# Optimization experiments

Hardware: AMD Instinct MI355X
Metric: run time of the kernel (lower is better)

## Reference

```python
import jax, jax.numpy as jnp
import numpy as np

DIM = 1024
HEADS = 16
HIDDEN = 4096
EPS = 1e-5


def layernorm(x, w, b):
    mu = jnp.mean(x, axis=-1, keepdims=True)
    var = jnp.var(x, axis=-1, keepdims=True)
    return (x - mu) * jax.lax.rsqrt(var + EPS) * w + b


def setup_inputs() -> dict:
    key = jax.random.key(0)
    ks = jax.random.split(key, 12)
    s = lambda fan_in: 1.0 / np.sqrt(fan_in)
    return {
        "x": jax.random.normal(ks[0], (8, 1024, DIM), dtype=jnp.float32),
        "norm1_w": jnp.ones((DIM,), jnp.float32),
        "norm1_b": jnp.zeros((DIM,), jnp.float32),
        "qkv_w": jax.random.uniform(ks[1], (3 * DIM, DIM), jnp.float32, -s(DIM), s(DIM)),
        "proj_w": jax.random.uniform(ks[2], (DIM, DIM), jnp.float32, -s(DIM), s(DIM)),
        "proj_b": jax.random.uniform(ks[3], (DIM,), jnp.float32, -s(DIM), s(DIM)),
        "norm2_w": jnp.ones((DIM,), jnp.float32),
        "norm2_b": jnp.zeros((DIM,), jnp.float32),
        "fc1_w": jax.random.uniform(ks[4], (HIDDEN, DIM), jnp.float32, -s(DIM), s(DIM)),
        "fc1_b": jax.random.uniform(ks[5], (HIDDEN,), jnp.float32, -s(DIM), s(DIM)),
        "fc2_w": jax.random.uniform(ks[6], (DIM, HIDDEN), jnp.float32, -s(HIDDEN), s(HIDDEN)),
        "fc2_b": jax.random.uniform(ks[7], (DIM,), jnp.float32, -s(HIDDEN), s(HIDDEN)),
    }


def reference(x, norm1_w, norm1_b, qkv_w, proj_w, proj_b,
              norm2_w, norm2_b, fc1_w, fc1_b, fc2_w, fc2_b):
    B, N, C = x.shape
    hd = C // HEADS
    scale = hd ** -0.5

    # ---- attention branch ----
    xn = layernorm(x, norm1_w, norm1_b)
    qkv_tmp = jnp.einsum('bnc,oc->bno', xn, qkv_w)          # [B,N,3C]
    qkv = qkv_tmp.reshape(B, N, 3, HEADS, hd).transpose(2, 0, 3, 1, 4)
    q, k, v = qkv[0], qkv[1], qkv[2]                         # [B,H,N,hd]
    qkv_out = qkv_tmp.reshape(B, N, 3, C).transpose(2, 0, 1, 3)
    attn = jnp.einsum('bhnd,bhmd->bhnm', q, k) * scale       # [B,H,N,N]
    attn = jax.nn.softmax(attn, axis=-1)
    ao = jnp.einsum('bhnm,bhmd->bhnd', attn, v)              # [B,H,N,hd]
    ao = ao.transpose(0, 2, 1, 3).reshape(B, N, C)
    attn_out = jnp.einsum('bnc,oc->bno', ao, proj_w) + proj_b
    x = x + attn_out

    # ---- mlp branch ----
    xn2 = layernorm(x, norm2_w, norm2_b)
    h = jnp.einsum('bnc,hc->bnh', xn2, fc1_w) + fc1_b
    h = jax.nn.gelu(h, approximate=False)
    hidden_out = jnp.einsum('bnh,ch->bnc', h, fc2_w) + fc2_b
    x = x + hidden_out
    return (x, (qkv_out[0], qkv_out[1], qkv_out[2]), hidden_out)
```

## Files before the change

### kernel.cpp

```cpp
#include <hip/hip_runtime.h>
#include <hip/hip_bf16.h>

typedef __attribute__((ext_vector_type(8))) __bf16 bf16x8;
typedef __attribute__((ext_vector_type(4))) float f32x4;
typedef unsigned short u16;
typedef unsigned int u32;

#define TOK 8192
#define C_DIM 1024
#define OUT_SEC 8388608

__device__ __forceinline__ u16 f2bf(float f) {
  return __builtin_bit_cast(u16, __float2bfloat16(f));
}

__device__ __forceinline__ int cvt_pk_bf16(float lo, float hi) {
  int r;
  asm("v_cvt_pk_bf16_f32 %0, %1, %2" : "=v"(r) : "v"(lo), "v"(hi));
  return r;
}

__device__ __forceinline__ float max3f(float a, float b, float c) {
  return fmaxf(fmaxf(a, b), c);
}

__device__ __forceinline__ void gl_lds16(const void* g, void* l) {
  __builtin_amdgcn_global_load_lds(
      (__attribute__((address_space(1))) void*)const_cast<void*>(g),
      (__attribute__((address_space(3))) void*)l, 16, 0, 0);
}

__device__ __forceinline__ float gelu_f(float x) {
  float y = 0.7978845608f * (x + 0.044715f * x * x * x);
  y = fminf(fmaxf(y, -15.f), 15.f);
  float e = __expf(2.0f * y);
  float th = (e - 1.0f) / (e + 1.0f);
  return 0.5f * x * (1.0f + th);
}

__global__ __launch_bounds__(256) void cvt_kernel(const float* __restrict__ in,
                                                  u16* __restrict__ out, int n4) {
  int i = blockIdx.x * blockDim.x + threadIdx.x;
  if (i >= n4) return;
  float4 v = reinterpret_cast<const float4*>(in)[i];
  alignas(8) u16 pk[4];
  pk[0] = f2bf(v.x); pk[1] = f2bf(v.y); pk[2] = f2bf(v.z); pk[3] = f2bf(v.w);
  reinterpret_cast<uint2*>(out)[i] = *reinterpret_cast<uint2*>(pk);
}

__global__ __launch_bounds__(256) void ln_kernel(const float* __restrict__ x,
                                                 const float* __restrict__ w,
                                                 const float* __restrict__ b,
                                                 u16* __restrict__ out) {
  const int row = blockIdx.x;
  const int t = threadIdx.x;
  const float* xr = x + (size_t)row * C_DIM;
  float4 v = reinterpret_cast<const float4*>(xr)[t];
  float s = v.x + v.y + v.z + v.w;
  float ss = v.x * v.x + v.y * v.y + v.z * v.z + v.w * v.w;
#pragma unroll
  for (int off = 1; off < 64; off <<= 1) {
    s += __shfl_xor(s, off, 64);
    ss += __shfl_xor(ss, off, 64);
  }
  __shared__ float red[8];
  const int wv = t >> 6;
  if ((t & 63) == 0) { red[wv] = s; red[4 + wv] = ss; }
  __syncthreads();
  s = red[0] + red[1] + red[2] + red[3];
  ss = red[4] + red[5] + red[6] + red[7];
  const float mu = s * (1.0f / C_DIM);
  const float var = ss * (1.0f / C_DIM) - mu * mu;
  const float rstd = rsqrtf(var + 1e-5f);
  float4 w4 = reinterpret_cast<const float4*>(w)[t];
  float4 b4 = reinterpret_cast<const float4*>(b)[t];
  alignas(8) u16 pk[4];
  pk[0] = f2bf((v.x - mu) * rstd * w4.x + b4.x);
  pk[1] = f2bf((v.y - mu) * rstd * w4.y + b4.y);
  pk[2] = f2bf((v.z - mu) * rstd * w4.z + b4.z);
  pk[3] = f2bf((v.w - mu) * rstd * w4.w + b4.w);
  reinterpret_cast<uint2*>(out + (size_t)row * C_DIM)[t] = *reinterpret_cast<uint2*>(pk);
}

__global__ __launch_bounds__(256) void vtrans_kernel(const float* __restrict__ vsrc,
                                                     u16* __restrict__ vt) {
  const int bh = blockIdx.x, nt = blockIdx.y;
  const int b = bh >> 4, h = bh & 15;
  const int t = threadIdx.x;
  __shared__ u16 T[64][65];
#pragma unroll
  for (int p = 0; p < 4; ++p) {
    const int idx = p * 256 + t;
    const int n = idx >> 4, d4 = (idx & 15) * 4;
    float4 x4 = *reinterpret_cast<const float4*>(
        vsrc + (size_t)(b * 1024 + nt * 64 + n) * 1024 + h * 64 + d4);
    T[d4 + 0][n] = f2bf(x4.x);
    T[d4 + 1][n] = f2bf(x4.y);
    T[d4 + 2][n] = f2bf(x4.z);
    T[d4 + 3][n] = f2bf(x4.w);
  }
  __syncthreads();
  const int d = t >> 2, ns = (t & 3) * 16;
  u16* dst = vt + (size_t)bh * 65536 + (size_t)d * 1024 + nt * 64 + ns;
  alignas(16) u16 tmp[16];
#pragma unroll
  for (int i = 0; i < 16; ++i) tmp[i] = T[d][ns + i];
  reinterpret_cast<uint4*>(dst)[0] = reinterpret_cast<uint4*>(tmp)[0];
  reinterpret_cast<uint4*>(dst)[1] = reinterpret_cast<uint4*>(tmp)[1];
}

#define MFMA_T(AF, BF, BASE)                                                \
  _Pragma("unroll") for (int nf = 0; nf < 4; ++nf) {                        \
    _Pragma("unroll") for (int mf = 0; mf < 4; ++mf)                        \
        acc[(BASE) + mf][nf] = __builtin_amdgcn_mfma_f32_16x16x32_bf16(     \
            AF[mf], BF[nf], acc[(BASE) + mf][nf], 0, 0, 0);                 \
  }

enum { EPIN_PROJ = 0, EPIN_FC2 = 1, EPIN_QKV = 2, EPIN_FC1 = 3 };

template <int EPI>
__global__ __launch_bounds__(512, 1) void gemm8n(
    const u16* __restrict__ A, const u16* __restrict__ Bw,
    const float* __restrict__ bias, const float* resid,
    float* out, float* out2_f, u16* __restrict__ h1, u16* __restrict__ h2,
    int K) {
  extern __shared__ char smem[];
  const int t = threadIdx.x, lane = t & 63, wid = t >> 6;
  const int wm = wid >> 2, wn = wid & 3;

  const int nwg = gridDim.x;
  int lin = blockIdx.x;
  lin = (lin & 7) * (nwg >> 3) + (lin >> 3);
  const int brow0 = (lin & 63) * 128;
  const int bcol0 = (lin >> 6) * 256;

  const int NT = K >> 6;

  f32x4 zero = {0.f, 0.f, 0.f, 0.f};
  f32x4 acc[4][4];
#pragma unroll
  for (int m = 0; m < 4; ++m)
#pragma unroll
    for (int n = 0; n < 4; ++n) acc[m][n] = zero;

  const int src_slot = ((t & 3) ^ ((t >> 3) & 3)) * 8;
  const int srow = t >> 2;
  auto stage_all = [&](char* dst, int ktile) {
#pragma unroll
    for (int ks = 0; ks < 2; ++ks) {
      const int k0 = ktile * 64 + ks * 32 + src_slot;
      gl_lds16(A + (size_t)(brow0 + srow) * K + k0, dst + ks * 8192 + t * 16);
    }
#pragma unroll
    for (int ks = 0; ks < 2; ++ks) {
      const int k0 = ktile * 64 + ks * 32 + src_slot;
      char* db = dst + 16384 + ks * 16384;
#pragma unroll
      for (int i = 0; i < 2; ++i)
        gl_lds16(Bw + (size_t)(bcol0 + i * 128 + srow) * K + k0, db + i * 8192 + t * 16);
    }
  };

  const int swz16 = (((lane >> 4) ^ ((lane >> 1) & 3)) << 4);
  const int l15 = lane & 15;

  char* bcur = smem;
  char* bnxt = smem + 49152;
  char* bspr = smem + 98304;

  stage_all(bcur, 0);
  stage_all(bnxt, 1);
  asm volatile("s_waitcnt vmcnt(6)" ::: "memory");
  __builtin_amdgcn_s_barrier();

  for (int tt = 0; tt < NT; ++tt) {
    const bool pf2 = (tt + 2 < NT);
    bf16x8 af[4], af2[4], bfr[4], bfr2[4];

    auto LDA = [&](bf16x8* dst8, int KK) {
#pragma unroll
      for (int mf = 0; mf < 4; ++mf)
        dst8[mf] = *reinterpret_cast<const bf16x8*>(
            bcur + KK * 8192 + (wm * 64 + mf * 16 + l15) * 64 + swz16);
    };
    auto LDB = [&](bf16x8* dst8, int KK) {
#pragma unroll
      for (int nf = 0; nf < 4; ++nf)
        dst8[nf] = *reinterpret_cast<const bf16x8*>(
            bcur + 16384 + KK * 16384 + (wn * 64 + nf * 16 + l15) * 64 + swz16);
    };

    LDA(af, 0);
    LDB(bfr, 0);
    __builtin_amdgcn_sched_barrier(0);
    LDA(af2, 1);
    LDB(bfr2, 1);
    __builtin_amdgcn_sched_barrier(0);
    if (pf2) stage_all(bspr, tt + 2);
    asm volatile("s_waitcnt lgkmcnt(8)" ::: "memory");
    __builtin_amdgcn_sched_barrier(0);
    __builtin_amdgcn_s_setprio(1);
    MFMA_T(af, bfr, 0)
    asm volatile("s_waitcnt lgkmcnt(0)" ::: "memory");
    __builtin_amdgcn_sched_barrier(0);
    MFMA_T(af2, bfr2, 0)
    __builtin_amdgcn_s_setprio(0);
    if (pf2) {
      asm volatile("s_waitcnt vmcnt(6)" ::: "memory");
    } else {
      asm volatile("s_waitcnt vmcnt(0)" ::: "memory");
    }
    __builtin_amdgcn_s_barrier();

    char* tmp = bcur;
    bcur = bnxt;
    bnxt = bspr;
    bspr = tmp;
  }

  const int rb = brow0 + wm * 64;
  const int cb = bcol0 + wn * 64;
#pragma unroll
  for (int m = 0; m < 4; ++m) {
#pragma unroll
    for (int n = 0; n < 4; ++n) {
      const int c = cb + n * 16 + l15;
#pragma unroll
      for (int j = 0; j < 4; ++j) {
        const int r = rb + m * 16 + (lane >> 4) * 4 + j;
        float v = acc[m][n][j];
        if constexpr (EPI == EPIN_PROJ) {
          v += bias[c] + resid[(size_t)r * 1024 + c];
          out[(size_t)r * 1024 + c] = v;
        } else if constexpr (EPI == EPIN_FC2) {
          v += bias[c];
          out[(size_t)r * 1024 + c] = v;
          out2_f[(size_t)r * 1024 + c] = resid[(size_t)r * 1024 + c] + v;
        } else if constexpr (EPI == EPIN_QKV) {
          const int sec = c >> 10, cc = c & 1023;
          out[(size_t)sec * OUT_SEC + (size_t)r * 1024 + cc] = v;
          const size_t boff =
              (((size_t)(r >> 10) * 16 + (cc >> 6)) * 1024 + (r & 1023)) * 64 + (cc & 63);
          if (sec == 0) h1[boff] = f2bf(v * 0.18033688f);
          else if (sec == 1) h2[boff] = f2bf(v);
        } else {
          v += bias[c];
          h1[(size_t)r * 4096 + c] = f2bf(gelu_f(v));
        }
      }
    }
  }
}

__global__ __launch_bounds__(256, 4) void attn_kernel(const u16* __restrict__ Qb,
                                                      const u16* __restrict__ Kb,
                                                      const u16* __restrict__ Vtb,
                                                      u16* __restrict__ ao) {
  const int orig = blockIdx.y * gridDim.x + blockIdx.x;
  const int wid = (orig & 7) * 128 + (orig >> 3);
  const int bh = wid >> 3;
  const int qt = wid & 7;
  const int b = bh >> 4, h = bh & 15;
  const int t = threadIdx.x, lane = t & 63, wv = t >> 6;
  const int l15 = lane & 15, g = lane >> 4;

  __shared__ u16 KV[2][8192];

  const int q0 = qt * 128 + wv * 32;
  bf16x8 qfA[2], qfB[2];
#pragma unroll
  for (int c = 0; c < 2; ++c) {
    qfA[c] = *reinterpret_cast<const bf16x8*>(
        Qb + (size_t)bh * 65536 + (size_t)(q0 + l15) * 64 + c * 32 + g * 8);
    qfB[c] = *reinterpret_cast<const bf16x8*>(
        Qb + (size_t)bh * 65536 + (size_t)(q0 + 16 + l15) * 64 + c * 32 + g * 8);
  }

  f32x4 zero = {0.f, 0.f, 0.f, 0.f};
  f32x4 accO0[4], accO1[4];
#pragma unroll
  for (int nb = 0; nb < 4; ++nb) { accO0[nb] = zero; accO1[nb] = zero; }
  float m0 = -1e30f, m1 = -1e30f, lr0 = 0.f, lr1 = 0.f;

  const char* ktile0 = (const char*)(Kb + (size_t)bh * 65536);
  const char* vbase = (const char*)(Vtb + (size_t)bh * 65536);

  auto stage = [&](int buf, int kv0) {
    char* base = (char*)KV[buf];
#pragma unroll
    for (int i = 0; i < 2; ++i) {
      const int o = i * 4096 + t * 16;
      const int row = o >> 7, colb = o & 127;
      const int swz = colb ^ ((row & 7) << 4);
      gl_lds16(ktile0 + (size_t)kv0 * 128 + (size_t)row * 128 + swz, base + o);
      gl_lds16(vbase + (size_t)row * 2048 + (size_t)kv0 * 2 + swz, base + 8192 + o);
    }
  };

  stage(0, 0);
  int cur = 0;

  const int a0 = (l15 + ((g & 1) << 5)) << 2;
  const int a1 = a0 + 64;
  const bool up = (lane & 32) != 0;

  for (int tile = 0; tile < 16; ++tile) {
    asm volatile("s_waitcnt vmcnt(0)" ::: "memory");
    __builtin_amdgcn_s_barrier();
    if (tile + 1 < 16) stage(cur ^ 1, (tile + 1) * 64);

    const char* kcur = (const char*)KV[cur];
    const char* vcur = kcur + 8192;

    f32x4 s0[4], s1[4];
#pragma unroll
    for (int jb = 0; jb < 4; ++jb) { s0[jb] = zero; s1[jb] = zero; }
#pragma unroll
    for (int jb = 0; jb < 4; ++jb)
#pragma unroll
      for (int c = 0; c < 2; ++c) {
        const int row = jb * 16 + l15;
        const int colb = c * 64 + g * 16;
        bf16x8 kf = *reinterpret_cast<const bf16x8*>(
            kcur + row * 128 + (colb ^ ((row & 7) << 4)));
        s0[jb] = __builtin_amdgcn_mfma_f32_16x16x32_bf16(kf, qfA[c], s0[jb], 0, 0, 0);
        s1[jb] = __builtin_amdgcn_mfma_f32_16x16x32_bf16(kf, qfB[c], s1[jb], 0, 0, 0);
      }

    int w0[4][2], w1[4][2];
    {
      float ta = max3f(s0[0][0], s0[0][1], s0[0][2]);
      float tb = max3f(s0[0][3], s0[1][0], s0[1][1]);
      float tc = max3f(s0[1][2], s0[1][3], s0[2][0]);
      float td = max3f(s0[2][1], s0[2][2], s0[2][3]);
      float te = max3f(s0[3][0], s0[3][1], s0[3][2]);
      float mt = max3f(max3f(ta, tb, tc), max3f(td, te, s0[3][3]), -1e30f);
      mt = fmaxf(mt, __shfl_xor(mt, 16, 64));
      mt = fmaxf(mt, __shfl_xor(mt, 32, 64));
      if (!__all(mt <= m0 + 8.0f)) {
        const float mn = fmaxf(m0, mt);
        const float sc = exp2f(m0 - mn);
        lr0 *= sc;
#pragma unroll
        for (int nb = 0; nb < 4; ++nb) accO0[nb] *= sc;
        m0 = mn;
      }
      float rs = 0.f;
#pragma unroll
      for (int jb = 0; jb < 4; ++jb)
#pragma unroll
        for (int r = 0; r < 4; ++r) {
          const float p = exp2f(s0[jb][r] - m0);
          s0[jb][r] = p;
          rs += p;
        }
      lr0 += rs;
#pragma unroll
      for (int jb = 0; jb < 4; ++jb) {
        w0[jb][0] = cvt_pk_bf16(s0[jb][0], s0[jb][1]);
        w0[jb][1] = cvt_pk_bf16(s0[jb][2], s0[jb][3]);
      }
    }
    {
      float ta = max3f(s1[0][0], s1[0][1], s1[0][2]);
      float tb = max3f(s1[0][3], s1[1][0], s1[1][1]);
      float tc = max3f(s1[1][2], s1[1][3], s1[2][0]);
      float td = max3f(s1[2][1], s1[2][2], s1[2][3]);
      float te = max3f(s1[3][0], s1[3][1], s1[3][2]);
      float mt = max3f(max3f(ta, tb, tc), max3f(td, te, s1[3][3]), -1e30f);
      mt = fmaxf(mt, __shfl_xor(mt, 16, 64));
      mt = fmaxf(mt, __shfl_xor(mt, 32, 64));
      if (!__all(mt <= m1 + 8.0f)) {
        const float mn = fmaxf(m1, mt);
        const float sc = exp2f(m1 - mn);
        lr1 *= sc;
#pragma unroll
        for (int nb = 0; nb < 4; ++nb) accO1[nb] *= sc;
        m1 = mn;
      }
      float rs = 0.f;
#pragma unroll
      for (int jb = 0; jb < 4; ++jb)
#pragma unroll
        for (int r = 0; r < 4; ++r) {
          const float p = exp2f(s1[jb][r] - m1);
          s1[jb][r] = p;
          rs += p;
        }
      lr1 += rs;
#pragma unroll
      for (int jb = 0; jb < 4; ++jb) {
        w1[jb][0] = cvt_pk_bf16(s1[jb][0], s1[jb][1]);
        w1[jb][1] = cvt_pk_bf16(s1[jb][2], s1[jb][3]);
      }
    }

#pragma unroll
    for (int c = 0; c < 2; ++c) {
      int p0w0 = __builtin_amdgcn_ds_bpermute(a0, w0[2 * c][0]);
      int p0w0h = __builtin_amdgcn_ds_bpermute(a0, w0[2 * c + 1][0]);
      int p0w1 = __builtin_amdgcn_ds_bpermute(a0, w0[2 * c][1]);
      int p0w1h = __builtin_amdgcn_ds_bpermute(a0, w0[2 * c + 1][1]);
      int p0w2 = __builtin_amdgcn_ds_bpermute(a1, w0[2 * c][0]);
      int p0w2h = __builtin_amdgcn_ds_bpermute(a1, w0[2 * c + 1][0]);
      int p0w3 = __builtin_amdgcn_ds_bpermute(a1, w0[2 * c][1]);
      int p0w3h = __builtin_amdgcn_ds_bpermute(a1, w0[2 * c + 1][1]);
      alignas(16) int word0[4] = {up ? p0w0h : p0w0, up ? p0w1h : p0w1,
                                  up ? p0w2h : p0w2, up ? p0w3h : p0w3};
      bf16x8 pf0 = *reinterpret_cast<bf16x8*>(word0);

      int p1w0 = __builtin_amdgcn_ds_bpermute(a0, w1[2 * c][0]);
      int p1w0h = __builtin_amdgcn_ds_bpermute(a0, w1[2 * c + 1][0]);
      int p1w1 = __builtin_amdgcn_ds_bpermute(a0, w1[2 * c][1]);
      int p1w1h = __builtin_amdgcn_ds_bpermute(a0, w1[2 * c + 1][1]);
      int p1w2 = __builtin_amdgcn_ds_bpermute(a1, w1[2 * c][0]);
      int p1w2h = __builtin_amdgcn_ds_bpermute(a1, w1[2 * c + 1][0]);
      int p1w3 = __builtin_amdgcn_ds_bpermute(a1, w1[2 * c][1]);
      int p1w3h = __builtin_amdgcn_ds_bpermute(a1, w1[2 * c + 1][1]);
      alignas(16) int word1[4] = {up ? p1w0h : p1w0, up ? p1w1h : p1w1,
                                  up ? p1w2h : p1w2, up ? p1w3h : p1w3};
      bf16x8 pf1 = *reinterpret_cast<bf16x8*>(word1);

#pragma unroll
      for (int nb = 0; nb < 4; ++nb) {
        const int row = nb * 16 + l15;
        const int colb = c * 64 + g * 16;
        bf16x8 vf = *reinterpret_cast<const bf16x8*>(
            vcur + row * 128 + (colb ^ ((row & 7) << 4)));
        accO0[nb] = __builtin_amdgcn_mfma_f32_16x16x32_bf16(vf, pf0, accO0[nb], 0, 0, 0);
        accO1[nb] = __builtin_amdgcn_mfma_f32_16x16x32_bf16(vf, pf1, accO1[nb], 0, 0, 0);
      }
    }

    cur ^= 1;
  }

  lr0 += __shfl_xor(lr0, 16, 64);
  lr0 += __shfl_xor(lr0, 32, 64);
  lr1 += __shfl_xor(lr1, 16, 64);
  lr1 += __shfl_xor(lr1, 32, 64);
  const float rl0 = __builtin_amdgcn_rcpf(lr0);
  const float rl1 = __builtin_amdgcn_rcpf(lr1);

  u16* dst0 = ao + (size_t)(b * 1024 + q0 + l15) * 1024 + h * 64 + g * 4;
  u16* dst1 = ao + (size_t)(b * 1024 + q0 + 16 + l15) * 1024 + h * 64 + g * 4;
#pragma unroll
  for (int nb = 0; nb < 4; ++nb) {
    alignas(8) u16 pk0[4], pk1[4];
#pragma unroll
    for (int j = 0; j < 4; ++j) {
      pk0[j] = f2bf(accO0[nb][j] * rl0);
      pk1[j] = f2bf(accO1[nb][j] * rl1);
    }
    *reinterpret_cast<uint2*>(dst0 + nb * 16) = *reinterpret_cast<uint2*>(pk0);
    *reinterpret_cast<uint2*>(dst1 + nb * 16) = *reinterpret_cast<uint2*>(pk1);
  }
}

extern "C" void kernel_launch(void* const* d_in, const int* in_sizes, int n_in,
                              void* d_out, int out_size, void* d_ws, size_t ws_size,
                              hipStream_t stream) {
  const float* x      = (const float*)d_in[0];
  const float* n1w    = (const float*)d_in[1];
  const float* n1b    = (const float*)d_in[2];
  const float* qkv_w  = (const float*)d_in[3];
  const float* proj_w = (const float*)d_in[4];
  const float* proj_b = (const float*)d_in[5];
  const float* n2w    = (const float*)d_in[6];
  const float* n2b    = (const float*)d_in[7];
  const float* fc1_w  = (const float*)d_in[8];
  const float* fc1_b  = (const float*)d_in[9];
  const float* fc2_w  = (const float*)d_in[10];
  const float* fc2_b  = (const float*)d_in[11];
  float* out = (float*)d_out;

  u16* wsb    = (u16*)d_ws;
  u16* w_qkv  = wsb;
  u16* w_proj = wsb + 3145728;
  u16* w_fc1  = wsb + 4194304;
  u16* w_fc2  = wsb + 8388608;
  u16* xn     = wsb + 12582912;
  u16* Qb     = wsb + 20971520;
  u16* Kb     = wsb + 29360128;
  u16* Vtw    = wsb + 37748736;
  u16* ao     = wsb + 46137344;
  u16* hbuf   = wsb + 20971520;

  (void)hipFuncSetAttribute((const void*)gemm8n<EPIN_PROJ>,
                            hipFuncAttributeMaxDynamicSharedMemorySize, 147456);
  (void)hipFuncSetAttribute((const void*)gemm8n<EPIN_FC2>,
                            hipFuncAttributeMaxDynamicSharedMemorySize, 147456);
  (void)hipFuncSetAttribute((const void*)gemm8n<EPIN_QKV>,
                            hipFuncAttributeMaxDynamicSharedMemorySize, 147456);
  (void)hipFuncSetAttribute((const void*)gemm8n<EPIN_FC1>,
                            hipFuncAttributeMaxDynamicSharedMemorySize, 147456);

  cvt_kernel<<<3072, 256, 0, stream>>>(qkv_w, w_qkv, 786432);
  cvt_kernel<<<1024, 256, 0, stream>>>(proj_w, w_proj, 262144);
  cvt_kernel<<<4096, 256, 0, stream>>>(fc1_w, w_fc1, 1048576);
  cvt_kernel<<<4096, 256, 0, stream>>>(fc2_w, w_fc2, 1048576);

  ln_kernel<<<TOK, 256, 0, stream>>>(x, n1w, n1b, xn);
  gemm8n<EPIN_QKV><<<768, 512, 147456, stream>>>(
      xn, w_qkv, nullptr, nullptr, out + OUT_SEC, nullptr, Qb, Kb, 1024);
  vtrans_kernel<<<dim3(128, 16), 256, 0, stream>>>(out + 3 * (size_t)OUT_SEC, Vtw);
  attn_kernel<<<dim3(128, 8), 256, 0, stream>>>(Qb, Kb, Vtw, ao);
  gemm8n<EPIN_PROJ><<<256, 512, 147456, stream>>>(
      ao, w_proj, proj_b, x, out, nullptr, nullptr, nullptr, 1024);
  ln_kernel<<<TOK, 256, 0, stream>>>(out, n2w, n2b, xn);
  gemm8n<EPIN_FC1><<<1024, 512, 147456, stream>>>(
      xn, w_fc1, fc1_b, nullptr, nullptr, nullptr, hbuf, nullptr, 1024);
  gemm8n<EPIN_FC2><<<256, 512, 147456, stream>>>(
      hbuf, w_fc2, fc2_b, out, out + 4 * (size_t)OUT_SEC, out, nullptr, nullptr, 4096);
}
```

Before: 419.3 us.

## Shrink GEMM tiles to 128x128 with 4-stage K32 pipeline and two blocks per CU

The GEMM block tile drops from 128x256 with 8 waves to 128x128 with 4 waves, and the K step drops from 64 to 32. The triple-buffered LDS pipeline becomes a 4-stage ring, prefetching three tiles ahead with 64 KB of LDS. Launch bounds now allow two blocks per CU, and grid sizes double. The aim is better latency hiding through higher occupancy and a deeper prefetch, at the cost of less operand reuse per block, more global traffic, and more barriers per unit of work.

Measured after the change: 464.8 us. +10.9%, slower.

```diff
diff --git a/kernel.cpp b/kernel.cpp
--- a/kernel.cpp
+++ b/kernel.cpp
@@ -119,22 +119,22 @@
 enum { EPIN_PROJ = 0, EPIN_FC2 = 1, EPIN_QKV = 2, EPIN_FC1 = 3 };
 
 template <int EPI>
-__global__ __launch_bounds__(512, 1) void gemm8n(
+__global__ __launch_bounds__(256, 2) void gemm8n(
     const u16* __restrict__ A, const u16* __restrict__ Bw,
     const float* __restrict__ bias, const float* resid,
     float* out, float* out2_f, u16* __restrict__ h1, u16* __restrict__ h2,
     int K) {
   extern __shared__ char smem[];
   const int t = threadIdx.x, lane = t & 63, wid = t >> 6;
-  const int wm = wid >> 2, wn = wid & 3;
+  const int wm = wid >> 1, wn = wid & 1;
 
   const int nwg = gridDim.x;
   int lin = blockIdx.x;
   lin = (lin & 7) * (nwg >> 3) + (lin >> 3);
   const int brow0 = (lin & 63) * 128;
-  const int bcol0 = (lin >> 6) * 256;
-
-  const int NT = K >> 6;
+  const int bcol0 = (lin >> 6) * 128;
+
+  const int NT = K >> 5;
 
   f32x4 zero = {0.f, 0.f, 0.f, 0.f};
   f32x4 acc[4][4];
@@ -146,76 +146,51 @@
   const int src_slot = ((t & 3) ^ ((t >> 3) & 3)) * 8;
   const int srow = t >> 2;
   auto stage_all = [&](char* dst, int ktile) {
-#pragma unroll
-    for (int ks = 0; ks < 2; ++ks) {
-      const int k0 = ktile * 64 + ks * 32 + src_slot;
-      gl_lds16(A + (size_t)(brow0 + srow) * K + k0, dst + ks * 8192 + t * 16);
-    }
-#pragma unroll
-    for (int ks = 0; ks < 2; ++ks) {
-      const int k0 = ktile * 64 + ks * 32 + src_slot;
-      char* db = dst + 16384 + ks * 16384;
-#pragma unroll
-      for (int i = 0; i < 2; ++i)
-        gl_lds16(Bw + (size_t)(bcol0 + i * 128 + srow) * K + k0, db + i * 8192 + t * 16);
-    }
+    const int k0 = ktile * 32 + src_slot;
+#pragma unroll
+    for (int i = 0; i < 2; ++i)
+      gl_lds16(A + (size_t)(brow0 + i * 64 + srow) * K + k0, dst + i * 4096 + t * 16);
+#pragma unroll
+    for (int i = 0; i < 2; ++i)
+      gl_lds16(Bw + (size_t)(bcol0 + i * 64 + srow) * K + k0, dst + 8192 + i * 4096 + t * 16);
   };
 
   const int swz16 = (((lane >> 4) ^ ((lane >> 1) & 3)) << 4);
   const int l15 = lane & 15;
 
-  char* bcur = smem;
-  char* bnxt = smem + 49152;
-  char* bspr = smem + 98304;
-
-  stage_all(bcur, 0);
-  stage_all(bnxt, 1);
-  asm volatile("s_waitcnt vmcnt(6)" ::: "memory");
+  stage_all(smem, 0);
+  stage_all(smem + 16384, 1);
+  stage_all(smem + 32768, 2);
+  asm volatile("s_waitcnt vmcnt(8)" ::: "memory");
   __builtin_amdgcn_s_barrier();
 
   for (int tt = 0; tt < NT; ++tt) {
-    const bool pf2 = (tt + 2 < NT);
-    bf16x8 af[4], af2[4], bfr[4], bfr2[4];
-
-    auto LDA = [&](bf16x8* dst8, int KK) {
-#pragma unroll
-      for (int mf = 0; mf < 4; ++mf)
-        dst8[mf] = *reinterpret_cast<const bf16x8*>(
-            bcur + KK * 8192 + (wm * 64 + mf * 16 + l15) * 64 + swz16);
-    };
-    auto LDB = [&](bf16x8* dst8, int KK) {
-#pragma unroll
-      for (int nf = 0; nf < 4; ++nf)
-        dst8[nf] = *reinterpret_cast<const bf16x8*>(
-            bcur + 16384 + KK * 16384 + (wn * 64 + nf * 16 + l15) * 64 + swz16);
-    };
-
-    LDA(af, 0);
-    LDB(bfr, 0);
+    char* bcur = smem + ((tt & 3) << 14);
+    bf16x8 af[4], bfr[4];
+
+#pragma unroll
+    for (int mf = 0; mf < 4; ++mf)
+      af[mf] = *reinterpret_cast<const bf16x8*>(
+          bcur + (wm * 64 + mf * 16 + l15) * 64 + swz16);
+#pragma unroll
+    for (int nf = 0; nf < 4; ++nf)
+      bfr[nf] = *reinterpret_cast<const bf16x8*>(
+          bcur + 8192 + (wn * 64 + nf * 16 + l15) * 64 + swz16);
     __builtin_amdgcn_sched_barrier(0);
-    LDA(af2, 1);
-    LDB(bfr2, 1);
-    __builtin_amdgcn_sched_barrier(0);
-    if (pf2) stage_all(bspr, tt + 2);
-    asm volatile("s_waitcnt lgkmcnt(8)" ::: "memory");
+    if (tt + 3 < NT) stage_all(smem + (((tt + 3) & 3) << 14), tt + 3);
+    asm volatile("s_waitcnt lgkmcnt(0)" ::: "memory");
     __builtin_amdgcn_sched_barrier(0);
     __builtin_amdgcn_s_setprio(1);
     MFMA_T(af, bfr, 0)
-    asm volatile("s_waitcnt lgkmcnt(0)" ::: "memory");
-    __builtin_amdgcn_sched_barrier(0);
-    MFMA_T(af2, bfr2, 0)
     __builtin_amdgcn_s_setprio(0);
-    if (pf2) {
-      asm volatile("s_waitcnt vmcnt(6)" ::: "memory");
+    if (tt + 3 < NT) {
+      asm volatile("s_waitcnt vmcnt(8)" ::: "memory");
+    } else if (tt + 2 < NT) {
+      asm volatile("s_waitcnt vmcnt(4)" ::: "memory");
     } else {
       asm volatile("s_waitcnt vmcnt(0)" ::: "memory");
     }
     __builtin_amdgcn_s_barrier();
-
-    char* tmp = bcur;
-    bcur = bnxt;
-    bnxt = bspr;
-    bspr = tmp;
   }
 
   const int rb = brow0 + wm * 64;
@@ -487,13 +462,13 @@
   u16* hbuf   = wsb + 20971520;
 
   (void)hipFuncSetAttribute((const void*)gemm8n<EPIN_PROJ>,
-                            hipFuncAttributeMaxDynamicSharedMemorySize, 147456);
+                            hipFuncAttributeMaxDynamicSharedMemorySize, 65536);
   (void)hipFuncSetAttribute((const void*)gemm8n<EPIN_FC2>,
-                            hipFuncAttributeMaxDynamicSharedMemorySize, 147456);
+                            hipFuncAttributeMaxDynamicSharedMemorySize, 65536);
   (void)hipFuncSetAttribute((const void*)gemm8n<EPIN_QKV>,
-                            hipFuncAttributeMaxDynamicSharedMemorySize, 147456);
+                            hipFuncAttributeMaxDynamicSharedMemorySize, 65536);
   (void)hipFuncSetAttribute((const void*)gemm8n<EPIN_FC1>,
-                            hipFuncAttributeMaxDynamicSharedMemorySize, 147456);
+                            hipFuncAttributeMaxDynamicSharedMemorySize, 65536);
 
   cvt_kernel<<<3072, 256, 0, stream>>>(qkv_w, w_qkv, 786432);
   cvt_kernel<<<1024, 256, 0, stream>>>(proj_w, w_proj, 262144);
@@ -501,15 +476,15 @@
   cvt_kernel<<<4096, 256, 0, stream>>>(fc2_w, w_fc2, 1048576);
 
   ln_kernel<<<TOK, 256, 0, stream>>>(x, n1w, n1b, xn);
-  gemm8n<EPIN_QKV><<<768, 512, 147456, stream>>>(
+  gemm8n<EPIN_QKV><<<1536, 256, 65536, stream>>>(
       xn, w_qkv, nullptr, nullptr, out + OUT_SEC, nullptr, Qb, Kb, 1024);
   vtrans_kernel<<<dim3(128, 16), 256, 0, stream>>>(out + 3 * (size_t)OUT_SEC, Vtw);
   attn_kernel<<<dim3(128, 8), 256, 0, stream>>>(Qb, Kb, Vtw, ao);
-  gemm8n<EPIN_PROJ><<<256, 512, 147456, stream>>>(
+  gemm8n<EPIN_PROJ><<<512, 256, 65536, stream>>>(
       ao, w_proj, proj_b, x, out, nullptr, nullptr, nullptr, 1024);
   ln_kernel<<<TOK, 256, 0, stream>>>(out, n2w, n2b, xn);
-  gemm8n<EPIN_FC1><<<1024, 512, 147456, stream>>>(
+  gemm8n<EPIN_FC1><<<2048, 256, 65536, stream>>>(
       xn, w_fc1, fc1_b, nullptr, nullptr, nullptr, hbuf, nullptr, 1024);
-  gemm8n<EPIN_FC2><<<256, 512, 147456, stream>>>(
+  gemm8n<EPIN_FC2><<<512, 256, 65536, stream>>>(
       hbuf, w_fc2, fc2_b, out, out + 4 * (size_t)OUT_SEC, out, nullptr, nullptr, 4096);
 }
```
